# Kernel optimization log

Hardware: AMD Instinct MI355X
Metric: run time of the kernel (lower is better)

## Reference

```python
import jax, jax.numpy as jnp
import numpy as np

EPSILON = 1e-6
MINMAX_RATIO = 20 ** 0.5
N_NODES, N_EDGES = 60000, 240000
WIDTH, NUM_HEAD, DIM_HEAD = 256, 8, 32
WIDTH_NORM = NUM_HEAD * DIM_HEAD          # 256
WIDTH_ACT = NUM_HEAD * DIM_HEAD * 4       # 1024
EDGE_VOCAB, EDGE_FEATS = 16, 3


def _inv_softplus(y):
    return np.log(np.expm1(y))


def setup_inputs() -> dict:
    key = jax.random.key(0)
    ks = jax.random.split(key, 16)
    inp = {
        'x': jax.random.normal(ks[0], (N_NODES, WIDTH), jnp.float32),
        'deg': jax.random.randint(ks[1], (N_NODES,), 0, 6, jnp.int32),
        'edge_idx': jax.random.randint(ks[2], (2, N_EDGES), 0, N_NODES, jnp.int32),
        'edge_attr': jax.random.randint(ks[3], (N_EDGES, EDGE_FEATS), 0, EDGE_VOCAB, jnp.int32),
        'node_elec': jax.random.normal(ks[4], (N_NODES, 2), jnp.float32),
        # parameters (init scales per module code)
        'lora_down': jax.random.normal(ks[5], (WIDTH, DIM_HEAD)) / np.sqrt(WIDTH),
        # original init is zeros; small random values used so this path is exercised
        'lora_up': jax.random.normal(ks[6], (DIM_HEAD, WIDTH_NORM)) * 0.01,
        'emb_edge': jax.random.normal(ks[7], (EDGE_VOCAB, DIM_HEAD)) * (0.01 / np.sqrt(EDGE_FEATS)),
        'moa_w': jnp.zeros((2, DIM_HEAD), jnp.float32),
        'moa_s': jnp.tile(jnp.linspace(float(_inv_softplus(0.1)), float(_inv_softplus(10.0)), DIM_HEAD), (2, 1)),
        'elec_lin': jax.random.normal(ks[8], (2, DIM_HEAD)) * (0.01 / np.sqrt(2)),
        'emb_deg': jax.random.normal(ks[9], (6, WIDTH_NORM)) * 0.1,
        'lin_pre': jax.random.normal(ks[10], (WIDTH, WIDTH_NORM)) / np.sqrt(WIDTH),
        'gate_lin': jax.random.normal(ks[11], (WIDTH_NORM, WIDTH_NORM)) / np.sqrt(WIDTH_NORM),
        'gate_kernel': jax.random.normal(ks[12], (NUM_HEAD, DIM_HEAD, DIM_HEAD * 4)) / np.sqrt(DIM_HEAD),
        'value_lin': jax.random.normal(ks[13], (WIDTH_NORM, WIDTH_NORM)) / np.sqrt(WIDTH_NORM),
        'value_kernel': jax.random.normal(ks[14], (NUM_HEAD, DIM_HEAD, DIM_HEAD * 4)) / np.sqrt(DIM_HEAD),
        'act_bias': jnp.full((WIDTH_ACT,), float(_inv_softplus(0.5)), jnp.float32),
        'post_kernel': jax.random.normal(ks[15], (NUM_HEAD, DIM_HEAD * 4, DIM_HEAD)) / np.sqrt(DIM_HEAD * 4),
    }
    return inp


def _clip_with_grad(x, lo, hi):
    return jax.lax.stop_gradient(jnp.clip(x, lo, hi) - x) + x


def _group_linear(x, lin_kernel, head_kernel, norm_bias=None):
    H, D, F = head_kernel.shape
    xx = (x @ lin_kernel).reshape(*x.shape[:-1], H, D)
    xx = xx / jnp.sqrt(jnp.mean(jnp.square(xx), axis=-1, keepdims=True) + EPSILON)
    if norm_bias is not None:
        xx = (xx + norm_bias.reshape(xx.shape)) / 2 ** 0.5
    xx = jnp.einsum('nhd,hdf->nhf', xx, head_kernel)
    return xx.reshape(*x.shape[:-1], H * F)


def reference(x, deg, edge_idx, edge_attr, node_elec, lora_down, lora_up, emb_edge,
              moa_w, moa_s, elec_lin, emb_deg, lin_pre, gate_lin, gate_kernel,
              value_lin, value_kernel, act_bias, post_kernel):
    ei0, ei1 = edge_idx[0], edge_idx[1]
    # edge embedding: bond features + electronegativity difference (MoAct tanh mixture)
    diff = node_elec[ei0] - node_elec[ei1]                      # [E,2]
    w = jax.nn.softplus(moa_w)
    w = w / w.sum(axis=-1, keepdims=True)
    s = jax.nn.softplus(moa_s)
    moa_out = (jnp.tanh(diff[..., None] * s) * w).sum(-1)       # [E,2]
    emb = jnp.sum(emb_edge[edge_attr], axis=-2) + moa_out @ elec_lin  # [E,dim_head]
    # per-edge message with LoRA modulation, scatter-add to destination nodes
    msg = x[ei0] + x[ei1]                                       # [E,width]
    msg = msg @ lin_pre + ((msg @ lora_down) * emb) @ lora_up   # [E,width_norm]
    agg = jax.ops.segment_sum(msg, ei1, num_segments=x.shape[0])
    # gated post-block with degree-embedding gate bias
    gate_bias = emb_deg[deg]                                    # [N,width_norm]
    gg = _group_linear(agg, gate_lin, gate_kernel, gate_bias)   # [N,width_act]
    vv = _group_linear(agg, value_lin, value_kernel)
    a = jax.nn.softplus(gg + act_bias)
    a = _clip_with_grad(a, 1.0 / MINMAX_RATIO, MINMAX_RATIO)
    xx = (a * vv).reshape(agg.shape[0], NUM_HEAD, -1)           # [N,H,4*dim_head]
    xx = jnp.einsum('nhd,hdf->nhf', xx, post_kernel)
    return xx.reshape(agg.shape[0], -1)                         # [N,width_norm]
```

## Files before the change

kernel.cpp:

```cpp
#include <hip/hip_runtime.h>
#include <hip/hip_bf16.h>

typedef unsigned short u16;

#define NN 60000
#define NE 240000

typedef __attribute__((ext_vector_type(8))) short bfrag;
typedef __attribute__((ext_vector_type(4))) float ffrag;

__device__ __forceinline__ float bf2f(u16 u) {
    union { unsigned int i; float f; } v; v.i = ((unsigned int)u) << 16; return v.f;
}
__device__ __forceinline__ u16 f2bf(float f) {
    __hip_bfloat16 h = __float2bfloat16(f);
    return *reinterpret_cast<u16*>(&h);
}
__device__ __forceinline__ float softplusf(float x) {
    return fmaxf(x, 0.f) + log1pf(expf(-fabsf(x)));
}
__device__ __forceinline__ float fast_softplus(float x) {
    return __logf(1.f + __expf(x));
}
__device__ __forceinline__ float fast_sp_clip(float x) {
    float a = __logf(1.f + __expf(x));
    return fminf(fmaxf(a, 0.22360679774997896f), 4.47213595499957939f);
}
__device__ __forceinline__ float fast_tanh(float x) {
    float t = __expf(fminf(fmaxf(2.f * x, -30.f), 30.f));
    return (t - 1.f) * __builtin_amdgcn_rcpf(t + 1.f);
}
template<bool B>
__device__ __forceinline__ float LD(const void* p, int i) {
    if constexpr (B) return bf2f(((const u16*)p)[i]);
    else             return ((const float*)p)[i];
}
__device__ __forceinline__ bfrag ldfrag(const u16* p) {
    return *reinterpret_cast<const bfrag*>(p);
}
__device__ __forceinline__ ffrag MFMA(bfrag a, bfrag b, ffrag c) {
    return __builtin_amdgcn_mfma_f32_16x16x32_bf16(a, b, c, 0, 0, 0);
}

__global__ void detect_kernel(const u16* __restrict__ x, int* __restrict__ flag) {
    __shared__ int cnt;
    if (threadIdx.x == 0) cnt = 0;
    __syncthreads();
    int c = 0;
    for (int i = threadIdx.x; i < 2048; i += 256) {
        u16 w = x[2 * i];
        int e = (w >> 7) & 0xFF;
        if (e >= 112 && e <= 143) c++;
    }
    atomicAdd(&cnt, c);
    __syncthreads();
    if (threadIdx.x == 0) *flag = (cnt > 1024) ? 1 : 0;
}

template<bool B>
__device__ void prep_body(const void* gate_lin, const void* value_lin,
    const void* lin_pre, const void* lora_down, const void* lora_up,
    const void* gate_kernel, const void* value_kernel, const void* post_kernel,
    u16* gT, u16* vT, u16* lpT, u16* ldT, u16* luT, u16* gkT, u16* vkT, u16* pkT,
    int tid, int stride)
{
    for (int i = tid; i < 65536; i += stride) {
        int n = i >> 8, k = i & 255;
        gT[i]  = f2bf(LD<B>(gate_lin,  k * 256 + n));
        vT[i]  = f2bf(LD<B>(value_lin, k * 256 + n));
        lpT[i] = f2bf(LD<B>(lin_pre,   k * 256 + n));
    }
    for (int i = tid; i < 8192; i += stride) {
        { int n = i >> 8, k = i & 255; ldT[i] = f2bf(LD<B>(lora_down, k * 32 + n)); }
        { int n = i >> 5, k = i & 31;  luT[i] = f2bf(LD<B>(lora_up,   k * 256 + n)); }
    }
    for (int i = tid; i < 32768; i += stride) {
        { int hf = i >> 5, d = i & 31, h = hf >> 7, f = hf & 127;
          gkT[i] = f2bf(LD<B>(gate_kernel,  h * 4096 + d * 128 + f));
          vkT[i] = f2bf(LD<B>(value_kernel, h * 4096 + d * 128 + f)); }
        { int hd = i >> 7, f = i & 127, h = hd >> 5, d2 = hd & 31;
          pkT[i] = f2bf(LD<B>(post_kernel, h * 4096 + f * 32 + d2)); }
    }
}
__global__ void prep_kernel(const void* gate_lin, const void* value_lin,
    const void* lin_pre, const void* lora_down, const void* lora_up,
    const void* gate_kernel, const void* value_kernel, const void* post_kernel,
    u16* gT, u16* vT, u16* lpT, u16* ldT, u16* luT, u16* gkT, u16* vkT, u16* pkT,
    const int* flag)
{
    int tid = blockIdx.x * blockDim.x + threadIdx.x;
    int stride = gridDim.x * blockDim.x;
    if (*flag) prep_body<true >(gate_lin, value_lin, lin_pre, lora_down, lora_up,
        gate_kernel, value_kernel, post_kernel, gT, vT, lpT, ldT, luT, gkT, vkT, pkT, tid, stride);
    else       prep_body<false>(gate_lin, value_lin, lin_pre, lora_down, lora_up,
        gate_kernel, value_kernel, post_kernel, gT, vT, lpT, ldT, luT, gkT, vkT, pkT, tid, stride);
}


struct PreSmem { __align__(16) u16 xB[64][264]; };

template<bool B>
__device__ void pre_body(PreSmem& sm, const void* x, const u16* lpT, const u16* ldT,
                         float* y, u16* xd, int blk, int j)
{
    const int w = j >> 6, quad = (j >> 4) & 3, l15 = j & 15;
    {
        int row = j >> 2, seg = j & 3, c0 = seg * 64;
        int gr = blk * 64 + row;
        if (gr < NN) {
            if constexpr (B) {
                const u16* xp = (const u16*)x + (size_t)gr * 256 + c0;
                for (int cc = 0; cc < 64; cc += 8)
                    *reinterpret_cast<bfrag*>(&sm.xB[row][c0 + cc]) = ldfrag(xp + cc);
            } else {
                const float* xp = (const float*)x + (size_t)gr * 256 + c0;
                for (int cc = 0; cc < 64; cc += 4) {
                    float4 v = *(const float4*)(xp + cc);
                    ushort4 o = { f2bf(v.x), f2bf(v.y), f2bf(v.z), f2bf(v.w) };
                    *reinterpret_cast<ushort4*>(&sm.xB[row][c0 + cc]) = o;
                }
            }
        } else {
            bfrag z = {0,0,0,0,0,0,0,0};
            for (int cc = 0; cc < 64; cc += 8)
                *reinterpret_cast<bfrag*>(&sm.xB[row][c0 + cc]) = z;
        }
    }
    __syncthreads();
    const int r0 = w * 16;
    bfrag A[8];
    #pragma unroll
    for (int kt = 0; kt < 8; kt++)
        A[kt] = ldfrag(&sm.xB[r0 + l15][kt * 32 + quad * 8]);

    for (int t = 0; t < 16; t++) {
        int n0 = t * 16;
        const u16* bp = lpT + (n0 + l15) * 256 + quad * 8;
        bfrag b0 = ldfrag(bp +   0), b1 = ldfrag(bp +  32),
              b2 = ldfrag(bp +  64), b3 = ldfrag(bp +  96),
              b4 = ldfrag(bp + 128), b5 = ldfrag(bp + 160),
              b6 = ldfrag(bp + 192), b7 = ldfrag(bp + 224);
        ffrag acc = {0.f, 0.f, 0.f, 0.f};
        acc = MFMA(A[0], b0, acc); acc = MFMA(A[1], b1, acc);
        acc = MFMA(A[2], b2, acc); acc = MFMA(A[3], b3, acc);
        acc = MFMA(A[4], b4, acc); acc = MFMA(A[5], b5, acc);
        acc = MFMA(A[6], b6, acc); acc = MFMA(A[7], b7, acc);
        #pragma unroll
        for (int r = 0; r < 4; r++) {
            int gr = blk * 64 + r0 + quad * 4 + r;
            if (gr < NN) y[(size_t)gr * 256 + n0 + l15] = acc[r];
        }
    }
    #pragma unroll
    for (int t = 0; t < 2; t++) {
        int n0 = t * 16;
        ffrag acc = {0.f, 0.f, 0.f, 0.f};
        #pragma unroll
        for (int kt = 0; kt < 8; kt++)
            acc = MFMA(A[kt], ldfrag(ldT + (n0 + l15) * 256 + kt * 32 + quad * 8), acc);
        #pragma unroll
        for (int r = 0; r < 4; r++) {
            int gr = blk * 64 + r0 + quad * 4 + r;
            if (gr < NN) xd[(size_t)gr * 32 + n0 + l15] = f2bf(acc[r]);
        }
    }
}
__global__ __launch_bounds__(256) void pre_kernel(const void* x, const u16* lpT,
    const u16* ldT, float* y, u16* xd, const int* flag)
{
    __shared__ PreSmem sm;
    const int j = threadIdx.x, blk = blockIdx.x;
    if (*flag) pre_body<true >(sm, x, lpT, ldT, y, xd, blk, j);
    else       pre_body<false>(sm, x, lpT, ldT, y, xd, blk, j);
}

__global__ __launch_bounds__(256) void hist_kernel(const int* __restrict__ edge_idx,
                                                   int* __restrict__ cnt)
{
    int e = blockIdx.x * blockDim.x + threadIdx.x;
    int stride = gridDim.x * blockDim.x;
    for (; e < NE; e += stride) atomicAdd(&cnt[edge_idx[NE + e]], 1);
}

__global__ __launch_bounds__(256) void scanA_kernel(const int* __restrict__ cnt,
                                                    int* __restrict__ bsum)
{
    __shared__ int sd[256];
    int b = blockIdx.x, j = threadIdx.x;
    int base = b * 1024 + j * 4;
    int s = 0;
    #pragma unroll
    for (int k = 0; k < 4; k++) { int i = base + k; if (i < NN) s += cnt[i]; }
    sd[j] = s; __syncthreads();
    for (int st = 128; st > 0; st >>= 1) {
        if (j < st) sd[j] += sd[j + st];
        __syncthreads();
    }
    if (j == 0) bsum[b] = sd[0];
}

__global__ __launch_bounds__(256) void scanB_kernel(const int* __restrict__ cnt,
    const int* __restrict__ bsum, int* __restrict__ off, int* __restrict__ cur)
{
    __shared__ int sd[256];
    int b = blockIdx.x, j = threadIdx.x;
    int pre = 0;
    for (int k = 0; k < b; k++) pre += bsum[k];
    int base = b * 1024 + j * 4;
    int c[4]; int tsum = 0;
    #pragma unroll
    for (int k = 0; k < 4; k++) { int i = base + k; c[k] = (i < NN) ? cnt[i] : 0; tsum += c[k]; }
    sd[j] = tsum; __syncthreads();
    for (int st = 1; st < 256; st <<= 1) {
        int v = (j >= st) ? sd[j - st] : 0;
        __syncthreads();
        sd[j] += v;
        __syncthreads();
    }
    int excl = sd[j] - tsum;
    int run = pre + excl;
    #pragma unroll
    for (int k = 0; k < 4; k++) {
        int i = base + k;
        if (i < NN) { off[i] = run; cur[i] = run; }
        run += c[k];
    }
}

struct EdgeWSmem {
    float wL[64], sL[64];
    float embT[512];
    float elT[64];
};

template<bool B>
__device__ void edgew_body(EdgeWSmem& sm, const int* edge_idx, const int* edge_attr,
    const void* node_elec, const void* emb_edge, const void* moa_w, const void* moa_s,
    const void* elec_lin, const u16* xd, u16* W, int* srcL, int* cur, int g, int j)
{
    if (j < 64) {
        int c = j >> 5;
        float sw = fast_softplus(LD<B>(moa_w, j));
        float tot = 0.f;
        #pragma unroll
        for (int d = 0; d < 32; d++) tot += fast_softplus(LD<B>(moa_w, c * 32 + d));
        sm.wL[j] = sw / tot;
        sm.sL[j] = fast_softplus(LD<B>(moa_s, j));
        sm.elT[j] = LD<B>(elec_lin, j);
    }
    for (int i = j; i < 512; i += 256) sm.embT[i] = LD<B>(emb_edge, i);
    __syncthreads();

    const int t = j & 3, s = j >> 2, e = g * 64 + s;
    const int a = edge_idx[e], b = edge_idx[NE + e];
    const int ch = t >> 1, dr = (t & 1) * 16;
    float df = LD<B>(node_elec, a * 2 + ch) - LD<B>(node_elec, b * 2 + ch);
    float part = 0.f;
    #pragma unroll
    for (int d = 0; d < 16; d++) {
        int dd = ch * 32 + dr + d;
        part += fast_tanh(df * sm.sL[dd]) * sm.wL[dd];
    }
    part += __shfl_xor(part, 1);
    int base = (j & 63) & ~3;
    float moa0 = __shfl(part, base + 0);
    float moa1 = __shfl(part, base + 2);

    int a0 = edge_attr[e * 3 + 0], a1 = edge_attr[e * 3 + 1], a2 = edge_attr[e * 3 + 2];
    int d0 = t * 8;
    bfrag va = ldfrag(xd + (size_t)a * 32 + d0);
    bfrag vb = ldfrag(xd + (size_t)b * 32 + d0);
    bfrag o;
    #pragma unroll
    for (int q = 0; q < 8; q++) {
        int d = d0 + q;
        float emb = sm.embT[a0 * 32 + d] + sm.embT[a1 * 32 + d] + sm.embT[a2 * 32 + d]
                  + moa0 * sm.elT[d] + moa1 * sm.elT[32 + d];
        o[q] = (short)f2bf((bf2f((u16)va[q]) + bf2f((u16)vb[q])) * emb);
    }
    int slot = 0;
    if (t == 0) slot = atomicAdd(&cur[b], 1);
    slot = __shfl(slot, base);
    if (t == 0) srcL[slot] = a;
    *reinterpret_cast<bfrag*>(W + (size_t)slot * 32 + d0) = o;
}

__global__ __launch_bounds__(256) void edgew_kernel(const int* edge_idx,
    const int* edge_attr, const void* node_elec, const void* emb_edge,
    const void* moa_w, const void* moa_s, const void* elec_lin,
    const u16* xd, u16* W, int* srcL, int* cur, const int* flag)
{
    __shared__ EdgeWSmem sm;
    const int j = threadIdx.x, g = blockIdx.x;
    if (*flag) edgew_body<true >(sm, edge_idx, edge_attr, node_elec, emb_edge,
                                 moa_w, moa_s, elec_lin, xd, W, srcL, cur, g, j);
    else       edgew_body<false>(sm, edge_idx, edge_attr, node_elec, emb_edge,
                                 moa_w, moa_s, elec_lin, xd, W, srcL, cur, g, j);
}

struct NodeSmemF {
    __align__(16) union U1 {
        u16 aggB[16][264];
        u16 ghatB[16][264];
    } u1;
    __align__(16) union U2 {
        struct P { float gF[16][260]; float vF[16][260]; } p;
        u16 xxB[16][1032];
    } u2;
    __align__(16) u16 vhatB[16][264];
    __align__(16) u16 uB[16][40];
    float grmsL[16][8], vrmsL[16][8];
    int degL[16];
    int offL[16], idgL[16];
};

template<bool B>
__device__ void node_body_f(NodeSmemF& sm, const float* y, const u16* Wb,
    const int* srcL, const int* off, const int* cnt, const int* deg,
    const void* emb_deg, const void* act_bias, const u16* gT, const u16* vT,
    const u16* gkT, const u16* vkT, const u16* pkT, const u16* luT,
    void* out, int blk, int j)
{
    const int w = j >> 6, quad = (j >> 4) & 3, l15 = j & 15;
    const int n0g = blk * 16;

    if (j < 16) {
        sm.degL[j] = deg[n0g + j];
        sm.offL[j] = off[n0g + j];
        sm.idgL[j] = cnt[n0g + j];
    }
    __syncthreads();

    {
        int s = j >> 4, dp = j & 15;
        int o = sm.offL[s], dg = sm.idgL[s];
        float u0 = 0.f, u1 = 0.f;
        for (int i = 0; i < dg; i++) {
            const u16* wr = Wb + (size_t)(o + i) * 32;
            u0 += bf2f(wr[dp]); u1 += bf2f(wr[dp + 16]);
        }
        sm.uB[s][dp] = f2bf(u0); sm.uB[s][dp + 16] = f2bf(u1);
    }

    {
        int row = j >> 4, c0 = (j & 15) * 16;
        int o = sm.offL[row], dg = sm.idgL[row];
        float acc[16];
        #pragma unroll
        for (int k = 0; k < 16; k++) acc[k] = 0.f;
        for (int i = 0; i < dg; i++) {
            int src = srcL[o + i];
            const float* yr = y + (size_t)src * 256 + c0;
            #pragma unroll
            for (int k = 0; k < 16; k += 4) {
                float4 v = *(const float4*)(yr + k);
                acc[k] += v.x; acc[k + 1] += v.y; acc[k + 2] += v.z; acc[k + 3] += v.w;
            }
        }
        {
            const float* yr = y + (size_t)(n0g + row) * 256 + c0;
            float fd = (float)dg;
            #pragma unroll
            for (int k = 0; k < 16; k += 4) {
                float4 v = *(const float4*)(yr + k);
                acc[k]     = fmaf(fd, v.x, acc[k]);
                acc[k + 1] = fmaf(fd, v.y, acc[k + 1]);
                acc[k + 2] = fmaf(fd, v.z, acc[k + 2]);
                acc[k + 3] = fmaf(fd, v.w, acc[k + 3]);
            }
        }
        #pragma unroll
        for (int k = 0; k < 16; k++) sm.u2.p.gF[row][c0 + k] = acc[k];
    }
    __syncthreads();

    {
        bfrag uA = ldfrag(&sm.uB[l15][quad * 8]);
        #pragma unroll
        for (int tt = 0; tt < 4; tt++) {
            int n0 = (w * 4 + tt) * 16;
            ffrag c;
            #pragma unroll
            for (int r = 0; r < 4; r++) c[r] = sm.u2.p.gF[quad * 4 + r][n0 + l15];
            ffrag o = MFMA(uA, ldfrag(luT + (n0 + l15) * 32 + quad * 8), c);
            #pragma unroll
            for (int r = 0; r < 4; r++)
                sm.u1.aggB[quad * 4 + r][n0 + l15] = f2bf(o[r]);
        }
    }
    __syncthreads();

    {
        bfrag A[8];
        #pragma unroll
        for (int kt = 0; kt < 8; kt++)
            A[kt] = ldfrag(&sm.u1.aggB[l15][kt * 32 + quad * 8]);
        const u16* WT = (w >> 1) ? vT : gT;
        float (*OF)[260] = (w >> 1) ? sm.u2.p.vF : sm.u2.p.gF;
        int half = (w & 1) * 128;
        #pragma unroll
        for (int t = 0; t < 8; t++) {
            int n0 = half + t * 16;
            const u16* bp = WT + (n0 + l15) * 256 + quad * 8;
            bfrag b0 = ldfrag(bp +   0), b1 = ldfrag(bp +  32),
                  b2 = ldfrag(bp +  64), b3 = ldfrag(bp +  96),
                  b4 = ldfrag(bp + 128), b5 = ldfrag(bp + 160),
                  b6 = ldfrag(bp + 192), b7 = ldfrag(bp + 224);
            ffrag acc = {0.f, 0.f, 0.f, 0.f};
            acc = MFMA(A[0], b0, acc); acc = MFMA(A[1], b1, acc);
            acc = MFMA(A[2], b2, acc); acc = MFMA(A[3], b3, acc);
            acc = MFMA(A[4], b4, acc); acc = MFMA(A[5], b5, acc);
            acc = MFMA(A[6], b6, acc); acc = MFMA(A[7], b7, acc);
            #pragma unroll
            for (int r = 0; r < 4; r++)
                OF[quad * 4 + r][n0 + l15] = acc[r];
        }
    }
    __syncthreads();

    if (j < 128) {
        int r = j >> 3, h = j & 7;
        float gs = 0.f, vs = 0.f;
        #pragma unroll
        for (int d = 0; d < 32; d++) {
            float g = sm.u2.p.gF[r][h * 32 + d]; gs = fmaf(g, g, gs);
            float v = sm.u2.p.vF[r][h * 32 + d]; vs = fmaf(v, v, vs);
        }
        sm.grmsL[r][h] = 1.f / sqrtf(gs * (1.f / 32.f) + 1e-6f);
        sm.vrmsL[r][h] = 1.f / sqrtf(vs * (1.f / 32.f) + 1e-6f);
    }
    __syncthreads();

    {
        int row = j >> 4, c0 = l15 * 16;
        int dg = sm.degL[row];
        float bias[16];
        if constexpr (B) {
            const u16* ep = (const u16*)emb_deg + dg * 256 + c0;
            bfrag e0 = ldfrag(ep), e1 = ldfrag(ep + 8);
            #pragma unroll
            for (int q = 0; q < 8; q++) {
                bias[q] = bf2f((u16)e0[q]); bias[q + 8] = bf2f((u16)e1[q]);
            }
        } else {
            const float* ep = (const float*)emb_deg + dg * 256 + c0;
            #pragma unroll
            for (int q = 0; q < 16; q += 4) {
                float4 v = *(const float4*)(ep + q);
                bias[q] = v.x; bias[q + 1] = v.y; bias[q + 2] = v.z; bias[q + 3] = v.w;
            }
        }
        float gi = sm.grmsL[row][c0 >> 5], vi = sm.vrmsL[row][c0 >> 5];
        #pragma unroll
        for (int cq = 0; cq < 16; cq += 2) {
            int c = c0 + cq;
            float v0 = sm.u2.p.vF[row][c] * vi;
            float v1 = sm.u2.p.vF[row][c + 1] * vi;
            float g0 = (sm.u2.p.gF[row][c] * gi + bias[cq]) * 0.70710678118654752f;
            float g1 = (sm.u2.p.gF[row][c + 1] * gi + bias[cq + 1]) * 0.70710678118654752f;
            unsigned int pv = (unsigned int)f2bf(v0) | ((unsigned int)f2bf(v1) << 16);
            unsigned int pg = (unsigned int)f2bf(g0) | ((unsigned int)f2bf(g1) << 16);
            *reinterpret_cast<unsigned int*>(&sm.vhatB[row][c]) = pv;
            *reinterpret_cast<unsigned int*>(&sm.u1.ghatB[row][c]) = pg;
        }
    }
    __syncthreads();

    #pragma unroll
    for (int hh = 0; hh < 2; hh++) {
        int h = w * 2 + hh;
        bfrag aG = ldfrag(&sm.u1.ghatB[l15][h * 32 + quad * 8]);
        bfrag aV = ldfrag(&sm.vhatB[l15][h * 32 + quad * 8]);
        #pragma unroll
        for (int t = 0; t < 8; t++) {
            int n0 = t * 16;
            bfrag bg = ldfrag(gkT + (h * 128 + n0 + l15) * 32 + quad * 8);
            bfrag bv = ldfrag(vkT + (h * 128 + n0 + l15) * 32 + quad * 8);
            ffrag zero = {0.f, 0.f, 0.f, 0.f};
            ffrag ag = MFMA(aG, bg, zero);
            ffrag av = MFMA(aV, bv, zero);
            int cc = h * 128 + n0 + l15;
            float bias = LD<B>(act_bias, cc);
            #pragma unroll
            for (int r = 0; r < 4; r++) {
                float a = fast_sp_clip(ag[r] + bias);
                sm.u2.xxB[quad * 4 + r][cc] = f2bf(a * av[r]);
            }
        }
    }
    __syncthreads();

    #pragma unroll
    for (int hh = 0; hh < 2; hh++) {
        int h = w * 2 + hh;
        bfrag A4[4];
        #pragma unroll
        for (int kt = 0; kt < 4; kt++)
            A4[kt] = ldfrag(&sm.u2.xxB[l15][h * 128 + kt * 32 + quad * 8]);
        #pragma unroll
        for (int t = 0; t < 2; t++) {
            int n0 = t * 16;
            const u16* pp = pkT + (h * 32 + n0 + l15) * 128 + quad * 8;
            bfrag c0 = ldfrag(pp), c1 = ldfrag(pp + 32),
                  c2 = ldfrag(pp + 64), c3 = ldfrag(pp + 96);
            ffrag acc = {0.f, 0.f, 0.f, 0.f};
            acc = MFMA(A4[0], c0, acc); acc = MFMA(A4[1], c1, acc);
            acc = MFMA(A4[2], c2, acc); acc = MFMA(A4[3], c3, acc);
            #pragma unroll
            for (int r = 0; r < 4; r++) {
                size_t idx = (size_t)(n0g + quad * 4 + r) * 256 + h * 32 + n0 + l15;
                if constexpr (B) ((u16*)out)[idx] = f2bf(acc[r]);
                else             ((float*)out)[idx] = acc[r];
            }
        }
    }
}

__global__ __launch_bounds__(256) void node_kernel_f(
    const float* y, const u16* Wb, const int* srcL, const int* off, const int* cnt,
    const int* deg, const void* emb_deg, const void* act_bias,
    const u16* gT, const u16* vT, const u16* gkT, const u16* vkT, const u16* pkT,
    const u16* luT, void* out, const int* flag)
{
    __shared__ NodeSmemF sm;
    const int j = threadIdx.x, blk = blockIdx.x;
    if (*flag) node_body_f<true >(sm, y, Wb, srcL, off, cnt, deg, emb_deg, act_bias,
                                  gT, vT, gkT, vkT, pkT, luT, out, blk, j);
    else       node_body_f<false>(sm, y, Wb, srcL, off, cnt, deg, emb_deg, act_bias,
                                  gT, vT, gkT, vkT, pkT, luT, out, blk, j);
}

struct EdgeSmemM {
    __align__(16) u16 msgB[64][264];
    __align__(16) u16 uB[64][40];
    __align__(16) float embL[64][32];
    float wL[64], sL[64];
    float moaL[64][2];
    int ei0s[64], ei1s[64];
};

template<bool B>
__device__ void edge_body_m(EdgeSmemM& sm, const void* x, const int* edge_idx,
    const int* edge_attr, const void* node_elec, const void* emb_edge,
    const void* moa_w, const void* moa_s, const void* elec_lin,
    const u16* ldT, const u16* luT, const u16* lpT, float* agg, int g, int j)
{
    const int w = j >> 6, quad = (j >> 4) & 3, l15 = j & 15;
    const int lane = j & 63;

    if (w == 0) {
        int c = lane >> 5;
        float sw = softplusf(LD<B>(moa_w, lane));
        float tot = 0.f;
        #pragma unroll
        for (int d = 0; d < 32; d++) tot += softplusf(LD<B>(moa_w, c * 32 + d));
        sm.wL[lane] = sw / tot;
        sm.sL[lane] = softplusf(LD<B>(moa_s, lane));
        int e = g * 64 + lane;
        int a = edge_idx[e], b = edge_idx[NE + e];
        sm.ei0s[lane] = a; sm.ei1s[lane] = b;
        #pragma unroll
        for (int c2 = 0; c2 < 2; c2++) {
            float df = LD<B>(node_elec, a * 2 + c2) - LD<B>(node_elec, b * 2 + c2);
            float acc = 0.f;
            for (int d = 0; d < 32; d++)
                acc += tanhf(df * sm.sL[c2 * 32 + d]) * sm.wL[c2 * 32 + d];
            sm.moaL[lane][c2] = acc;
        }
    }
    __syncthreads();

    {
        int row = j >> 2, seg = j & 3, c0 = seg * 64;
        int e0 = sm.ei0s[row], e1 = sm.ei1s[row];
        if constexpr (B) {
            const u16* xp = (const u16*)x;
            for (int cc = 0; cc < 64; cc += 8) {
                bfrag v0 = ldfrag(xp + (size_t)e0 * 256 + c0 + cc);
                bfrag v1 = ldfrag(xp + (size_t)e1 * 256 + c0 + cc);
                bfrag o;
                #pragma unroll
                for (int q = 0; q < 8; q++)
                    o[q] = (short)f2bf(bf2f((u16)v0[q]) + bf2f((u16)v1[q]));
                *reinterpret_cast<bfrag*>(&sm.msgB[row][c0 + cc]) = o;
            }
        } else {
            const float* xp = (const float*)x;
            for (int cc = 0; cc < 64; cc += 4) {
                float4 v0 = *(const float4*)(xp + (size_t)e0 * 256 + c0 + cc);
                float4 v1 = *(const float4*)(xp + (size_t)e1 * 256 + c0 + cc);
                ushort4 o = { f2bf(v0.x + v1.x), f2bf(v0.y + v1.y),
                              f2bf(v0.z + v1.z), f2bf(v0.w + v1.w) };
                *reinterpret_cast<ushort4*>(&sm.msgB[row][c0 + cc]) = o;
            }
        }
        int e = row, d0 = seg * 8, ea = g * 64 + e;
        int a0 = edge_attr[ea * 3 + 0], a1 = edge_attr[ea * 3 + 1], a2 = edge_attr[ea * 3 + 2];
        float m0 = sm.moaL[e][0], m1 = sm.moaL[e][1];
        #pragma unroll
        for (int d = d0; d < d0 + 8; d++) {
            sm.embL[e][d] = LD<B>(emb_edge, a0 * 32 + d) + LD<B>(emb_edge, a1 * 32 + d)
                          + LD<B>(emb_edge, a2 * 32 + d)
                          + m0 * LD<B>(elec_lin, d) + m1 * LD<B>(elec_lin, 32 + d);
        }
    }
    __syncthreads();

    const int r0 = w * 16;
    bfrag A[8];
    #pragma unroll
    for (int kt = 0; kt < 8; kt++)
        A[kt] = ldfrag(&sm.msgB[r0 + l15][kt * 32 + quad * 8]);

    #pragma unroll
    for (int t = 0; t < 2; t++) {
        int n0 = t * 16;
        ffrag acc = {0.f, 0.f, 0.f, 0.f};
        #pragma unroll
        for (int kt = 0; kt < 8; kt++)
            acc = MFMA(A[kt], ldfrag(ldT + (n0 + l15) * 256 + kt * 32 + quad * 8), acc);
        #pragma unroll
        for (int r = 0; r < 4; r++) {
            int row = r0 + quad * 4 + r;
            sm.uB[row][n0 + l15] = f2bf(acc[r] * sm.embL[row][n0 + l15]);
        }
    }
    bfrag uA = ldfrag(&sm.uB[r0 + l15][quad * 8]);

    int er[4];
    #pragma unroll
    for (int r = 0; r < 4; r++) er[r] = sm.ei1s[r0 + quad * 4 + r];

    for (int t = 0; t < 16; t++) {
        int n0 = t * 16;
        ffrag acc = {0.f, 0.f, 0.f, 0.f};
        #pragma unroll
        for (int kt = 0; kt < 8; kt++)
            acc = MFMA(A[kt], ldfrag(lpT + (n0 + l15) * 256 + kt * 32 + quad * 8), acc);
        acc = MFMA(uA, ldfrag(luT + (n0 + l15) * 32 + quad * 8), acc);
        #pragma unroll
        for (int r = 0; r < 4; r++)
            unsafeAtomicAdd(&agg[(size_t)er[r] * 256 + n0 + l15], acc[r]);
    }
}

__global__ __launch_bounds__(256) void edge_kernel_m(
    const void* x, const int* edge_idx, const int* edge_attr,
    const void* node_elec, const void* emb_edge, const void* moa_w,
    const void* moa_s, const void* elec_lin,
    const u16* ldT, const u16* luT, const u16* lpT, float* agg, const int* flag)
{
    __shared__ EdgeSmemM sm;
    const int j = threadIdx.x, g = blockIdx.x;
    if (*flag) edge_body_m<true >(sm, x, edge_idx, edge_attr, node_elec, emb_edge,
                                  moa_w, moa_s, elec_lin, ldT, luT, lpT, agg, g, j);
    else       edge_body_m<false>(sm, x, edge_idx, edge_attr, node_elec, emb_edge,
                                  moa_w, moa_s, elec_lin, ldT, luT, lpT, agg, g, j);
}

struct NodeSmemM {
    union U1 {
        u16 aggB[16][264];
        u16 ghatB[16][264];
    } u1;
    union U2 {
        struct P { float gF[16][260]; float vF[16][260]; } p;
        u16 xxB[16][1032];
    } u2;
    __align__(16) u16 vhatB[16][264];
    float grmsL[16][8], vrmsL[16][8];
    int degL[16];
};

template<bool B>
__device__ void node_body_m(NodeSmemM& sm, const float* agg, const int* deg,
    const void* emb_deg, const void* act_bias, const u16* gT, const u16* vT,
    const u16* gkT, const u16* vkT, const u16* pkT, void* out, int blk, int j)
{
    const int w = j >> 6, quad = (j >> 4) & 3, l15 = j & 15;
    const int n0g = blk * 16;

    {
// ... 205 lines not shown
    for (int s = 0; s < 8; s++)
        unsafeAtomicAdd(&agg[(size_t)sm.ei1s[s] * 256 + j], acc[s]);
}

__global__ __launch_bounds__(256) void edge_kernel_fb(
    const void* x, const int* edge_idx, const int* edge_attr,
    const void* node_elec, const void* lora_down, const void* lora_up,
    const void* emb_edge, const void* moa_w, const void* moa_s,
    const void* elec_lin, const void* lin_pre, float* agg, const int* flag)
{
    __shared__ EdgeSmemFB sm;
    const int j = threadIdx.x, g = blockIdx.x;
    if (*flag) edge_body_fb<true >(sm, x, edge_idx, edge_attr, node_elec, lora_down,
                                   lora_up, emb_edge, moa_w, moa_s, elec_lin, lin_pre, agg, g, j);
    else       edge_body_fb<false>(sm, x, edge_idx, edge_attr, node_elec, lora_down,
                                   lora_up, emb_edge, moa_w, moa_s, elec_lin, lin_pre, agg, g, j);
}

struct NodeSmemFB {
    __align__(16) float aggT[256][8];
    float gL[8][256];
    float vL[8][256];
    float ghat[256], vhat[256];
    float xxL[1024];
};

template<bool B>
__device__ void node_body_fb(NodeSmemFB& sm,
    const float* agg, const int* deg, const void* emb_deg,
    const void* gate_lin, const void* value_lin, const void* gate_kernel,
    const void* value_kernel, const void* act_bias, const void* post_kernel,
    void* out, int n0, int j)
{
    #pragma unroll
    for (int s = 0; s < 8; s++) sm.aggT[j][s] = agg[(size_t)(n0 + s) * 256 + j];
    __syncthreads();

    float ga[8], va[8];
    #pragma unroll
    for (int s = 0; s < 8; s++) { ga[s] = 0.f; va[s] = 0.f; }
    #pragma unroll 4
    for (int k = 0; k < 256; k++) {
        float wg = LD<B>(gate_lin,  k * 256 + j);
        float wv = LD<B>(value_lin, k * 256 + j);
        const float4 a0 = *reinterpret_cast<const float4*>(&sm.aggT[k][0]);
        const float4 a1 = *reinterpret_cast<const float4*>(&sm.aggT[k][4]);
        ga[0] = fmaf(a0.x, wg, ga[0]); va[0] = fmaf(a0.x, wv, va[0]);
        ga[1] = fmaf(a0.y, wg, ga[1]); va[1] = fmaf(a0.y, wv, va[1]);
        ga[2] = fmaf(a0.z, wg, ga[2]); va[2] = fmaf(a0.z, wv, va[2]);
        ga[3] = fmaf(a0.w, wg, ga[3]); va[3] = fmaf(a0.w, wv, va[3]);
        ga[4] = fmaf(a1.x, wg, ga[4]); va[4] = fmaf(a1.x, wv, va[4]);
        ga[5] = fmaf(a1.y, wg, ga[5]); va[5] = fmaf(a1.y, wv, va[5]);
        ga[6] = fmaf(a1.z, wg, ga[6]); va[6] = fmaf(a1.z, wv, va[6]);
        ga[7] = fmaf(a1.w, wg, ga[7]); va[7] = fmaf(a1.w, wv, va[7]);
    }
    __syncthreads();
    #pragma unroll
    for (int s = 0; s < 8; s++) { sm.gL[s][j] = ga[s]; sm.vL[s][j] = va[s]; }

    const int h = j >> 5, dd = j & 31, f0 = dd << 2;
    const float lo = 0.22360679774997896f, hi = 4.47213595499957939f;

    for (int s = 0; s < 8; s++) {
        __syncthreads();
        float gs = 0.f, vs = 0.f;
        #pragma unroll
        for (int d = 0; d < 32; d++) {
            float g = sm.gL[s][h * 32 + d];
            float v = sm.vL[s][h * 32 + d];
            gs = fmaf(g, g, gs); vs = fmaf(v, v, vs);
        }
        float grms = sqrtf(gs * (1.f / 32.f) + 1e-6f);
        float vrms = sqrtf(vs * (1.f / 32.f) + 1e-6f);
        float gv = sm.gL[s][j], vv = sm.vL[s][j];
        float bias = LD<B>(emb_deg, deg[n0 + s] * 256 + j);
        sm.ghat[j] = (gv / grms + bias) * 0.70710678118654752f;
        sm.vhat[j] = vv / vrms;
        __syncthreads();

        float a0 = 0.f, a1 = 0.f, a2 = 0.f, a3 = 0.f;
        float b0 = 0.f, b1 = 0.f, b2 = 0.f, b3 = 0.f;
        #pragma unroll 4
        for (int d = 0; d < 32; d++) {
            float gh = sm.ghat[h * 32 + d];
            float vh = sm.vhat[h * 32 + d];
            int base = h * 4096 + d * 128 + f0;
            a0 = fmaf(gh, LD<B>(gate_kernel,  base + 0), a0);
            a1 = fmaf(gh, LD<B>(gate_kernel,  base + 1), a1);
            a2 = fmaf(gh, LD<B>(gate_kernel,  base + 2), a2);
            a3 = fmaf(gh, LD<B>(gate_kernel,  base + 3), a3);
            b0 = fmaf(vh, LD<B>(value_kernel, base + 0), b0);
            b1 = fmaf(vh, LD<B>(value_kernel, base + 1), b1);
            b2 = fmaf(vh, LD<B>(value_kernel, base + 2), b2);
            b3 = fmaf(vh, LD<B>(value_kernel, base + 3), b3);
        }
        int fb = h * 128 + f0;
        a0 = fminf(fmaxf(softplusf(a0 + LD<B>(act_bias, fb + 0)), lo), hi);
        a1 = fminf(fmaxf(softplusf(a1 + LD<B>(act_bias, fb + 1)), lo), hi);
        a2 = fminf(fmaxf(softplusf(a2 + LD<B>(act_bias, fb + 2)), lo), hi);
        a3 = fminf(fmaxf(softplusf(a3 + LD<B>(act_bias, fb + 3)), lo), hi);
        sm.xxL[fb + 0] = a0 * b0; sm.xxL[fb + 1] = a1 * b1;
        sm.xxL[fb + 2] = a2 * b2; sm.xxL[fb + 3] = a3 * b3;
        __syncthreads();

        float o = 0.f;
        #pragma unroll 4
        for (int f = 0; f < 128; f++)
            o = fmaf(sm.xxL[h * 128 + f], LD<B>(post_kernel, h * 4096 + f * 32 + dd), o);
        if constexpr (B) ((u16*)out)[(size_t)(n0 + s) * 256 + j] = f2bf(o);
        else             ((float*)out)[(size_t)(n0 + s) * 256 + j] = o;
    }
}

__global__ __launch_bounds__(256) void node_kernel_fb(
    const float* agg, const int* deg, const void* emb_deg,
    const void* gate_lin, const void* value_lin, const void* gate_kernel,
    const void* value_kernel, const void* act_bias, const void* post_kernel,
    void* out, const int* flag)
{
    __shared__ NodeSmemFB sm;
    const int j = threadIdx.x, n0 = blockIdx.x * 8;
    if (*flag) node_body_fb<true >(sm, agg, deg, emb_deg, gate_lin, value_lin,
                                   gate_kernel, value_kernel, act_bias, post_kernel, out, n0, j);
    else       node_body_fb<false>(sm, agg, deg, emb_deg, gate_lin, value_lin,
                                   gate_kernel, value_kernel, act_bias, post_kernel, out, n0, j);
}

extern "C" void kernel_launch(void* const* d_in, const int* in_sizes, int n_in,
                              void* d_out, int out_size, void* d_ws, size_t ws_size,
                              hipStream_t stream) {
    const void* x           = d_in[0];
    const int*  deg         = (const int*)d_in[1];
    const int*  edge_idx    = (const int*)d_in[2];
    const int*  edge_attr   = (const int*)d_in[3];
    const void* node_elec   = d_in[4];
    const void* lora_down   = d_in[5];
    const void* lora_up     = d_in[6];
    const void* emb_edge    = d_in[7];
    const void* moa_w       = d_in[8];
    const void* moa_s       = d_in[9];
    const void* elec_lin    = d_in[10];
    const void* emb_deg     = d_in[11];
    const void* lin_pre     = d_in[12];
    const void* gate_lin    = d_in[13];
    const void* gate_kernel = d_in[14];
    const void* value_lin   = d_in[15];
    const void* value_kernel= d_in[16];
    const void* act_bias    = d_in[17];
    const void* post_kernel = d_in[18];

    const size_t AGG_BYTES = (size_t)NN * 256 * 4;
    const size_t T_BYTES   = (size_t)(3 * 65536 + 2 * 8192 + 3 * 32768) * 2;

    const size_t Y_OFF   = 16 + T_BYTES;
    const size_t W_OFF   = Y_OFF   + (size_t)NN * 256 * 4;
    const size_t XD_OFF  = W_OFF   + (size_t)NE * 32 * 2;
    const size_t SRC_OFF = XD_OFF  + (size_t)NN * 32 * 2;
    const size_t CNT_OFF = SRC_OFF + (size_t)NE * 4;
    const size_t OFF_OFF = CNT_OFF + (size_t)NN * 4;
    const size_t CUR_OFF = OFF_OFF + (size_t)NN * 4;
    const size_t BS_OFF  = CUR_OFF + (size_t)NN * 4;
    const size_t NEW_NEEDED = BS_OFF + 256;

    const size_t T_OFF_OLD  = AGG_BYTES + 16;
    const size_t OLD_NEEDED = T_OFF_OLD + T_BYTES;

    if (ws_size >= NEW_NEEDED) {
        int* flag = (int*)d_ws;
        u16* gT  = (u16*)((char*)d_ws + 16);
        u16* vT  = gT  + 65536;
        u16* lpT = vT  + 65536;
        u16* ldT = lpT + 65536;
        u16* luT = ldT + 8192;
        u16* gkT = luT + 8192;
        u16* vkT = gkT + 32768;
        u16* pkT = vkT + 32768;
        float* y   = (float*)((char*)d_ws + Y_OFF);
        u16*  Wb   = (u16*)((char*)d_ws + W_OFF);
        u16*  xd   = (u16*)((char*)d_ws + XD_OFF);
        int* srcL  = (int*)((char*)d_ws + SRC_OFF);
        int* cnt   = (int*)((char*)d_ws + CNT_OFF);
        int* offA  = (int*)((char*)d_ws + OFF_OFF);
        int* cur   = (int*)((char*)d_ws + CUR_OFF);
        int* bsum  = (int*)((char*)d_ws + BS_OFF);

        detect_kernel<<<1, 256, 0, stream>>>((const u16*)x, flag);
        prep_kernel<<<128, 256, 0, stream>>>(
            gate_lin, value_lin, lin_pre, lora_down, lora_up,
            gate_kernel, value_kernel, post_kernel,
            gT, vT, lpT, ldT, luT, gkT, vkT, pkT, flag);
        hipMemsetAsync(cnt, 0, (size_t)NN * 4, stream);
        pre_kernel<<<(NN + 63) / 64, 256, 0, stream>>>(x, lpT, ldT, y, xd, flag);
        hist_kernel<<<256, 256, 0, stream>>>(edge_idx, cnt);
        scanA_kernel<<<59, 256, 0, stream>>>(cnt, bsum);
        scanB_kernel<<<59, 256, 0, stream>>>(cnt, bsum, offA, cur);
        edgew_kernel<<<NE / 64, 256, 0, stream>>>(
            edge_idx, edge_attr, node_elec, emb_edge, moa_w, moa_s, elec_lin,
            xd, Wb, srcL, cur, flag);
        node_kernel_f<<<NN / 16, 256, 0, stream>>>(
            y, Wb, srcL, offA, cnt, deg, emb_deg, act_bias,
            gT, vT, gkT, vkT, pkT, luT, d_out, flag);
    } else if (ws_size >= OLD_NEEDED) {
        float* agg = (float*)d_ws;
        int* flag  = (int*)((char*)d_ws + AGG_BYTES);
        u16* gT  = (u16*)((char*)d_ws + T_OFF_OLD);
        u16* vT  = gT  + 65536;
        u16* lpT = vT  + 65536;
        u16* ldT = lpT + 65536;
        u16* luT = ldT + 8192;
        u16* gkT = luT + 8192;
        u16* vkT = gkT + 32768;
        u16* pkT = vkT + 32768;

        hipMemsetAsync(agg, 0, AGG_BYTES, stream);
        detect_kernel<<<1, 256, 0, stream>>>((const u16*)x, flag);
        prep_kernel<<<128, 256, 0, stream>>>(
            gate_lin, value_lin, lin_pre, lora_down, lora_up,
            gate_kernel, value_kernel, post_kernel,
            gT, vT, lpT, ldT, luT, gkT, vkT, pkT, flag);
        edge_kernel_m<<<NE / 64, 256, 0, stream>>>(
            x, edge_idx, edge_attr, node_elec, emb_edge, moa_w, moa_s, elec_lin,
            ldT, luT, lpT, agg, flag);
        node_kernel_m<<<NN / 16, 256, 0, stream>>>(
            agg, deg, emb_deg, act_bias, gT, vT, gkT, vkT, pkT, d_out, flag);
    } else {
        float* agg = (float*)d_ws;
        int* flag  = (int*)((char*)d_ws + AGG_BYTES);
        hipMemsetAsync(agg, 0, AGG_BYTES, stream);
        detect_kernel<<<1, 256, 0, stream>>>((const u16*)x, flag);
        edge_kernel_fb<<<NE / 8, 256, 0, stream>>>(
            x, edge_idx, edge_attr, node_elec, lora_down, lora_up, emb_edge,
            moa_w, moa_s, elec_lin, lin_pre, agg, flag);
        node_kernel_fb<<<NN / 8, 256, 0, stream>>>(
            agg, deg, emb_deg, gate_lin, value_lin, gate_kernel, value_kernel,
            act_bias, post_kernel, d_out, flag);
    }
}
```

Before: 490.3 us.

## Aggregate bf16 inputs per node before projecting through lin_pre

Instead of projecting every node through lin_pre up front and gathering fp32 projected rows per edge, the pre kernel now only writes a bf16 copy of x. The node kernel gathers and sums bf16 x rows, stages the source indices in shared memory, then runs the lin_pre projection once on the aggregated rows fused with the LoRA up-projection MFMA. This halves gather bytes (bf16 instead of fp32) and drops the large y buffer write. In exchange, the sum is rounded to bf16 before the matmul, which changes numerics slightly.

```diff
diff --git a/kernel.cpp b/kernel.cpp
--- a/kernel.cpp
+++ b/kernel.cpp
@@ -100,8 +100,8 @@
 struct PreSmem { __align__(16) u16 xB[64][264]; };
 
 template<bool B>
-__device__ void pre_body(PreSmem& sm, const void* x, const u16* lpT, const u16* ldT,
-                         float* y, u16* xd, int blk, int j)
+__device__ void pre_body(PreSmem& sm, const void* x, const u16* ldT,
+                         u16* xb, u16* xd, int blk, int j)
 {
     const int w = j >> 6, quad = (j >> 4) & 3, l15 = j & 15;
     {
@@ -114,10 +114,17 @@
                     *reinterpret_cast<bfrag*>(&sm.xB[row][c0 + cc]) = ldfrag(xp + cc);
             } else {
                 const float* xp = (const float*)x + (size_t)gr * 256 + c0;
-                for (int cc = 0; cc < 64; cc += 4) {
-                    float4 v = *(const float4*)(xp + cc);
-                    ushort4 o = { f2bf(v.x), f2bf(v.y), f2bf(v.z), f2bf(v.w) };
-                    *reinterpret_cast<ushort4*>(&sm.xB[row][c0 + cc]) = o;
+                u16* xbp = xb + (size_t)gr * 256 + c0;
+                for (int cc = 0; cc < 64; cc += 8) {
+                    float4 v0 = *(const float4*)(xp + cc);
+                    float4 v1 = *(const float4*)(xp + cc + 4);
+                    bfrag o;
+                    o[0] = (short)f2bf(v0.x); o[1] = (short)f2bf(v0.y);
+                    o[2] = (short)f2bf(v0.z); o[3] = (short)f2bf(v0.w);
+                    o[4] = (short)f2bf(v1.x); o[5] = (short)f2bf(v1.y);
+                    o[6] = (short)f2bf(v1.z); o[7] = (short)f2bf(v1.w);
+                    *reinterpret_cast<bfrag*>(&sm.xB[row][c0 + cc]) = o;
+                    *reinterpret_cast<bfrag*>(xbp + cc) = o;
                 }
             }
         } else {
@@ -133,24 +140,6 @@
     for (int kt = 0; kt < 8; kt++)
         A[kt] = ldfrag(&sm.xB[r0 + l15][kt * 32 + quad * 8]);
 
-    for (int t = 0; t < 16; t++) {
-        int n0 = t * 16;
-        const u16* bp = lpT + (n0 + l15) * 256 + quad * 8;
-        bfrag b0 = ldfrag(bp +   0), b1 = ldfrag(bp +  32),
-              b2 = ldfrag(bp +  64), b3 = ldfrag(bp +  96),
-              b4 = ldfrag(bp + 128), b5 = ldfrag(bp + 160),
-              b6 = ldfrag(bp + 192), b7 = ldfrag(bp + 224);
-        ffrag acc = {0.f, 0.f, 0.f, 0.f};
-        acc = MFMA(A[0], b0, acc); acc = MFMA(A[1], b1, acc);
-        acc = MFMA(A[2], b2, acc); acc = MFMA(A[3], b3, acc);
-        acc = MFMA(A[4], b4, acc); acc = MFMA(A[5], b5, acc);
-        acc = MFMA(A[6], b6, acc); acc = MFMA(A[7], b7, acc);
-        #pragma unroll
-        for (int r = 0; r < 4; r++) {
-            int gr = blk * 64 + r0 + quad * 4 + r;
-            if (gr < NN) y[(size_t)gr * 256 + n0 + l15] = acc[r];
-        }
-    }
     #pragma unroll
     for (int t = 0; t < 2; t++) {
         int n0 = t * 16;
@@ -165,13 +154,13 @@
         }
     }
 }
-__global__ __launch_bounds__(256) void pre_kernel(const void* x, const u16* lpT,
-    const u16* ldT, float* y, u16* xd, const int* flag)
+__global__ __launch_bounds__(256) void pre_kernel(const void* x, const u16* ldT,
+    u16* xb, u16* xd, const int* flag)
 {
     __shared__ PreSmem sm;
     const int j = threadIdx.x, blk = blockIdx.x;
-    if (*flag) pre_body<true >(sm, x, lpT, ldT, y, xd, blk, j);
-    else       pre_body<false>(sm, x, lpT, ldT, y, xd, blk, j);
+    if (*flag) pre_body<true >(sm, x, ldT, xb, xd, blk, j);
+    else       pre_body<false>(sm, x, ldT, xb, xd, blk, j);
 }
 
 __global__ __launch_bounds__(256) void hist_kernel(const int* __restrict__ edge_idx,
@@ -307,23 +296,27 @@
         struct P { float gF[16][260]; float vF[16][260]; } p;
         u16 xxB[16][1032];
     } u2;
-    __align__(16) u16 vhatB[16][264];
+    __align__(16) u16 sB[16][264];
     __align__(16) u16 uB[16][40];
     float grmsL[16][8], vrmsL[16][8];
-    int degL[16];
-    int offL[16], idgL[16];
+    int degL[16], offL[16], idgL[16];
+    int srcC[128];
 };
 
 template<bool B>
-__device__ void node_body_f(NodeSmemF& sm, const float* y, const u16* Wb,
-    const int* srcL, const int* off, const int* cnt, const int* deg,
+__device__ void node_body_f(NodeSmemF& sm, const void* x, const u16* xb,
+    const u16* Wb, const int* srcL, const int* off, const int* cnt, const int* deg,
     const void* emb_deg, const void* act_bias, const u16* gT, const u16* vT,
-    const u16* gkT, const u16* vkT, const u16* pkT, const u16* luT,
+    const u16* gkT, const u16* vkT, const u16* pkT, const u16* lpT, const u16* luT,
     void* out, int blk, int j)
 {
     const int w = j >> 6, quad = (j >> 4) & 3, l15 = j & 15;
     const int n0g = blk * 16;
-
+    const u16* xbp = B ? (const u16*)x : xb;
+
+    int o0 = off[n0g];
+    int eb = off[n0g + 15] + cnt[n0g + 15] - o0;
+    if (j < 128 && j < eb) sm.srcC[j] = srcL[o0 + j];
     if (j < 16) {
         sm.degL[j] = deg[n0g + j];
         sm.offL[j] = off[n0g + j];
@@ -332,60 +325,68 @@
     __syncthreads();
 
     {
-        int s = j >> 4, dp = j & 15;
-        int o = sm.offL[s], dg = sm.idgL[s];
+        int s = j >> 4, dp = j & 15, c0 = dp * 16;
+        int o = sm.offL[s], dg = sm.idgL[s], base = o - o0;
+        float acc[16];
+        #pragma unroll
+        for (int k = 0; k < 16; k++) acc[k] = 0.f;
         float u0 = 0.f, u1 = 0.f;
         for (int i = 0; i < dg; i++) {
-            const u16* wr = Wb + (size_t)(o + i) * 32;
-            u0 += bf2f(wr[dp]); u1 += bf2f(wr[dp + 16]);
+            int idx = base + i;
+            int src = (idx < 128) ? sm.srcC[idx] : srcL[o + i];
+            const u16* xr = xbp + (size_t)src * 256 + c0;
+            bfrag v0 = ldfrag(xr), v1 = ldfrag(xr + 8);
+            const u16* wr = Wb + (size_t)(o + i) * 32 + dp;
+            u0 += bf2f(wr[0]); u1 += bf2f(wr[16]);
+            #pragma unroll
+            for (int q = 0; q < 8; q++) {
+                acc[q]     += bf2f((u16)v0[q]);
+                acc[q + 8] += bf2f((u16)v1[q]);
+            }
+        }
+        {
+            const u16* xr = xbp + (size_t)(n0g + s) * 256 + c0;
+            bfrag v0 = ldfrag(xr), v1 = ldfrag(xr + 8);
+            float fd = (float)dg;
+            #pragma unroll
+            for (int q = 0; q < 8; q++) {
+                acc[q]     = fmaf(fd, bf2f((u16)v0[q]), acc[q]);
+                acc[q + 8] = fmaf(fd, bf2f((u16)v1[q]), acc[q + 8]);
+            }
         }
         sm.uB[s][dp] = f2bf(u0); sm.uB[s][dp + 16] = f2bf(u1);
-    }
+        #pragma unroll
+        for (int cq = 0; cq < 16; cq += 2) {
+            unsigned int pv = (unsigned int)f2bf(acc[cq]) | ((unsigned int)f2bf(acc[cq + 1]) << 16);
+            *reinterpret_cast<unsigned int*>(&sm.sB[s][c0 + cq]) = pv;
+        }
+    }
+    __syncthreads();
 
     {
-        int row = j >> 4, c0 = (j & 15) * 16;
-        int o = sm.offL[row], dg = sm.idgL[row];
-        float acc[16];
-        #pragma unroll
-        for (int k = 0; k < 16; k++) acc[k] = 0.f;
-        for (int i = 0; i < dg; i++) {
-            int src = srcL[o + i];
-            const float* yr = y + (size_t)src * 256 + c0;
-            #pragma unroll
-            for (int k = 0; k < 16; k += 4) {
-                float4 v = *(const float4*)(yr + k);
-                acc[k] += v.x; acc[k + 1] += v.y; acc[k + 2] += v.z; acc[k + 3] += v.w;
-            }
-        }
-        {
-            const float* yr = y + (size_t)(n0g + row) * 256 + c0;
-            float fd = (float)dg;
-            #pragma unroll
-            for (int k = 0; k < 16; k += 4) {
-                float4 v = *(const float4*)(yr + k);
-                acc[k]     = fmaf(fd, v.x, acc[k]);
-                acc[k + 1] = fmaf(fd, v.y, acc[k + 1]);
-                acc[k + 2] = fmaf(fd, v.z, acc[k + 2]);
-                acc[k + 3] = fmaf(fd, v.w, acc[k + 3]);
-            }
-        }
-        #pragma unroll
-        for (int k = 0; k < 16; k++) sm.u2.p.gF[row][c0 + k] = acc[k];
-    }
-    __syncthreads();
-
-    {
+        bfrag S[8];
+        #pragma unroll
+        for (int kt = 0; kt < 8; kt++)
+            S[kt] = ldfrag(&sm.sB[l15][kt * 32 + quad * 8]);
         bfrag uA = ldfrag(&sm.uB[l15][quad * 8]);
         #pragma unroll
         for (int tt = 0; tt < 4; tt++) {
             int n0 = (w * 4 + tt) * 16;
-            ffrag c;
-            #pragma unroll
-            for (int r = 0; r < 4; r++) c[r] = sm.u2.p.gF[quad * 4 + r][n0 + l15];
-            ffrag o = MFMA(uA, ldfrag(luT + (n0 + l15) * 32 + quad * 8), c);
+            const u16* bp = lpT + (n0 + l15) * 256 + quad * 8;
+            bfrag b0 = ldfrag(bp +   0), b1 = ldfrag(bp +  32),
+                  b2 = ldfrag(bp +  64), b3 = ldfrag(bp +  96),
+                  b4 = ldfrag(bp + 128), b5 = ldfrag(bp + 160),
+                  b6 = ldfrag(bp + 192), b7 = ldfrag(bp + 224);
+            bfrag lu = ldfrag(luT + (n0 + l15) * 32 + quad * 8);
+            ffrag acc = {0.f, 0.f, 0.f, 0.f};
+            acc = MFMA(S[0], b0, acc); acc = MFMA(S[1], b1, acc);
+            acc = MFMA(S[2], b2, acc); acc = MFMA(S[3], b3, acc);
+            acc = MFMA(S[4], b4, acc); acc = MFMA(S[5], b5, acc);
+            acc = MFMA(S[6], b6, acc); acc = MFMA(S[7], b7, acc);
+            acc = MFMA(uA, lu, acc);
             #pragma unroll
             for (int r = 0; r < 4; r++)
-                sm.u1.aggB[quad * 4 + r][n0 + l15] = f2bf(o[r]);
+                sm.u1.aggB[quad * 4 + r][n0 + l15] = f2bf(acc[r]);
         }
     }
     __syncthreads();
@@ -460,7 +461,7 @@
             float g1 = (sm.u2.p.gF[row][c + 1] * gi + bias[cq + 1]) * 0.70710678118654752f;
             unsigned int pv = (unsigned int)f2bf(v0) | ((unsigned int)f2bf(v1) << 16);
             unsigned int pg = (unsigned int)f2bf(g0) | ((unsigned int)f2bf(g1) << 16);
-            *reinterpret_cast<unsigned int*>(&sm.vhatB[row][c]) = pv;
+            *reinterpret_cast<unsigned int*>(&sm.sB[row][c]) = pv;
             *reinterpret_cast<unsigned int*>(&sm.u1.ghatB[row][c]) = pg;
         }
     }
@@ -470,7 +471,7 @@
     for (int hh = 0; hh < 2; hh++) {
         int h = w * 2 + hh;
         bfrag aG = ldfrag(&sm.u1.ghatB[l15][h * 32 + quad * 8]);
-        bfrag aV = ldfrag(&sm.vhatB[l15][h * 32 + quad * 8]);
+        bfrag aV = ldfrag(&sm.sB[l15][h * 32 + quad * 8]);
         #pragma unroll
         for (int t = 0; t < 8; t++) {
             int n0 = t * 16;
@@ -517,17 +518,17 @@
 }
 
 __global__ __launch_bounds__(256) void node_kernel_f(
-    const float* y, const u16* Wb, const int* srcL, const int* off, const int* cnt,
-    const int* deg, const void* emb_deg, const void* act_bias,
+    const void* x, const u16* xb, const u16* Wb, const int* srcL, const int* off,
+    const int* cnt, const int* deg, const void* emb_deg, const void* act_bias,
     const u16* gT, const u16* vT, const u16* gkT, const u16* vkT, const u16* pkT,
-    const u16* luT, void* out, const int* flag)
+    const u16* lpT, const u16* luT, void* out, const int* flag)
 {
     __shared__ NodeSmemF sm;
     const int j = threadIdx.x, blk = blockIdx.x;
-    if (*flag) node_body_f<true >(sm, y, Wb, srcL, off, cnt, deg, emb_deg, act_bias,
-                                  gT, vT, gkT, vkT, pkT, luT, out, blk, j);
-    else       node_body_f<false>(sm, y, Wb, srcL, off, cnt, deg, emb_deg, act_bias,
-                                  gT, vT, gkT, vkT, pkT, luT, out, blk, j);
+    if (*flag) node_body_f<true >(sm, x, xb, Wb, srcL, off, cnt, deg, emb_deg, act_bias,
+                                  gT, vT, gkT, vkT, pkT, lpT, luT, out, blk, j);
+    else       node_body_f<false>(sm, x, xb, Wb, srcL, off, cnt, deg, emb_deg, act_bias,
+                                  gT, vT, gkT, vkT, pkT, lpT, luT, out, blk, j);
 }
 
 struct EdgeSmemM {
@@ -1039,8 +1040,8 @@
     const size_t AGG_BYTES = (size_t)NN * 256 * 4;
     const size_t T_BYTES   = (size_t)(3 * 65536 + 2 * 8192 + 3 * 32768) * 2;
 
-    const size_t Y_OFF   = 16 + T_BYTES;
-    const size_t W_OFF   = Y_OFF   + (size_t)NN * 256 * 4;
+    const size_t XB_OFF  = 16 + T_BYTES;
+    const size_t W_OFF   = XB_OFF  + (size_t)NN * 256 * 2;
     const size_t XD_OFF  = W_OFF   + (size_t)NE * 32 * 2;
     const size_t SRC_OFF = XD_OFF  + (size_t)NN * 32 * 2;
     const size_t CNT_OFF = SRC_OFF + (size_t)NE * 4;
@@ -1062,7 +1063,7 @@
         u16* gkT = luT + 8192;
         u16* vkT = gkT + 32768;
         u16* pkT = vkT + 32768;
-        float* y   = (float*)((char*)d_ws + Y_OFF);
+        u16*  xb   = (u16*)((char*)d_ws + XB_OFF);
         u16*  Wb   = (u16*)((char*)d_ws + W_OFF);
         u16*  xd   = (u16*)((char*)d_ws + XD_OFF);
         int* srcL  = (int*)((char*)d_ws + SRC_OFF);
@@ -1077,7 +1078,7 @@
             gate_kernel, value_kernel, post_kernel,
             gT, vT, lpT, ldT, luT, gkT, vkT, pkT, flag);
         hipMemsetAsync(cnt, 0, (size_t)NN * 4, stream);
-        pre_kernel<<<(NN + 63) / 64, 256, 0, stream>>>(x, lpT, ldT, y, xd, flag);
+        pre_kernel<<<(NN + 63) / 64, 256, 0, stream>>>(x, ldT, xb, xd, flag);
         hist_kernel<<<256, 256, 0, stream>>>(edge_idx, cnt);
         scanA_kernel<<<59, 256, 0, stream>>>(cnt, bsum);
         scanB_kernel<<<59, 256, 0, stream>>>(cnt, bsum, offA, cur);
@@ -1085,8 +1086,8 @@
             edge_idx, edge_attr, node_elec, emb_edge, moa_w, moa_s, elec_lin,
             xd, Wb, srcL, cur, flag);
         node_kernel_f<<<NN / 16, 256, 0, stream>>>(
-            y, Wb, srcL, offA, cnt, deg, emb_deg, act_bias,
-            gT, vT, gkT, vkT, pkT, luT, d_out, flag);
+            x, xb, Wb, srcL, offA, cnt, deg, emb_deg, act_bias,
+            gT, vT, gkT, vkT, pkT, lpT, luT, d_out, flag);
     } else if (ws_size >= OLD_NEEDED) {
         float* agg = (float*)d_ws;
         int* flag  = (int*)((char*)d_ws + AGG_BYTES);
```

Result: no change. 492.4 us (+0.4%).
